# Optimization experiments

Measured on AMD Instinct MI355X. Metric: run time of the kernel, lower is better.

## Reference

```python
import jax, jax.numpy as jnp
import numpy as np

DOMAIN_MIN, DOMAIN_MAX = -1.0, 1.0
N, D_IN, D_OUT, K = 1024, 128, 128, 8


def setup_inputs() -> dict:
    key = jax.random.key(0)
    k1, k2, k3 = jax.random.split(key, 3)
    x = jax.random.uniform(k1, (N, D_IN), dtype=jnp.float32,
                           minval=DOMAIN_MIN, maxval=DOMAIN_MAX)
    # Per-edge spline knot values: near-identity init plus small noise.
    base = jnp.linspace(DOMAIN_MIN, DOMAIN_MAX, K, dtype=jnp.float32)
    coeffs = base[None, None, :] + 0.1 * jax.random.normal(
        k2, (D_OUT, D_IN, K), dtype=jnp.float32)
    weights = jax.random.normal(k3, (D_OUT, D_IN), dtype=jnp.float32) * np.sqrt(2.0 / D_IN)
    bias = jnp.zeros((D_OUT,), dtype=jnp.float32)
    return {"x": x, "coeffs": coeffs, "weights": weights, "bias": bias}


def _spline_all_edges(x, coeffs):
    """Evaluate every edge's cubic (Catmull-Rom) spline at its input.
    x: [N, d_in]; coeffs: [d_out, d_in, K] knot values on uniform knots in [-1,1].
    Returns s: [N, d_in, d_out]."""
    K_ = coeffs.shape[-1]
    h = (DOMAIN_MAX - DOMAIN_MIN) / (K_ - 1)
    xc = jnp.clip(x, DOMAIN_MIN, DOMAIN_MAX)
    t = (xc - DOMAIN_MIN) / h                      # [N, d_in], in [0, K-1]
    idx = jnp.clip(jnp.floor(t).astype(jnp.int32), 0, K_ - 2)
    u = t - idx                                    # local coord in [0,1]
    i0 = jnp.clip(idx - 1, 0, K_ - 1)
    i1 = idx
    i2 = idx + 1
    i3 = jnp.clip(idx + 2, 0, K_ - 1)
    ct = jnp.transpose(coeffs, (1, 2, 0))          # [d_in, K, d_out]
    jar = jnp.arange(ct.shape[0])[None, :]          # [1, d_in]
    p0 = ct[jar, i0]                               # [N, d_in, d_out]
    p1 = ct[jar, i1]
    p2 = ct[jar, i2]
    p3 = ct[jar, i3]
    u2 = u * u
    u3 = u2 * u
    b0 = 0.5 * (-u3 + 2.0 * u2 - u)
    b1 = 0.5 * (3.0 * u3 - 5.0 * u2 + 2.0)
    b2 = 0.5 * (-3.0 * u3 + 4.0 * u2 + u)
    b3 = 0.5 * (u3 - u2)
    return (b0[..., None] * p0 + b1[..., None] * p1 +
            b2[..., None] * p2 + b3[..., None] * p3)


def reference(x, coeffs, weights, bias):
    # h_i(x) = sum_j w_ij * s_ij(x_j) + b_i
    s = _spline_all_edges(x, coeffs)               # [N, d_in, d_out]
    return jnp.einsum('njo,oj->no', s, weights) + bias[None, :]
```

## Files before the change

kernel.cpp:

```cpp
#include <hip/hip_runtime.h>
#include <hip/hip_bf16.h>
#include <stdint.h>


#define DIN 128
#define DOUT 128
#define KTOT 1024
#define MT 16
#define PADW 1032

typedef unsigned int u32;
typedef unsigned short u16;
typedef __attribute__((ext_vector_type(8))) short bf16x8;
typedef __attribute__((ext_vector_type(4))) float f32x4;

union H8 { u16 s[8]; uint4 v; };

__device__ __forceinline__ u16 f2b(float f) {
    union { __hip_bfloat16 h; u16 u; } c;
    c.h = __float2bfloat16(f);
    return c.u;
}

__global__ __launch_bounds__(512) void kan_mfma(
    const float* __restrict__ x, const float* __restrict__ coeffs,
    const float* __restrict__ weights, const float* __restrict__ bias,
    float* __restrict__ out)
{
    __shared__ __align__(16) u16 sA[MT * PADW];
    __shared__ float sC[8 * 256];

    const int tid  = threadIdx.x;
    const int wave = tid >> 6;
    const int lane = tid & 63;
    const int n0 = blockIdx.x * MT;
    const int og = blockIdx.y * 32;

    #pragma unroll
    for (int it = 0; it < 4; ++it) {
        const int task = tid + it * 512;
        const int row = task >> 7;
        const int j = task & 127;
        float xv = x[(n0 + row) * DIN + j];
        xv = fminf(fmaxf(xv, -1.0f), 1.0f);
        const float t = (xv + 1.0f) * 3.5f;
        int idx = (int)t; idx = idx > 6 ? 6 : idx;
        const float u = t - (float)idx;
        const float u2 = u * u, u3 = u2 * u;
        const float b0 = 0.5f * (-u3 + 2.0f * u2 - u);
        const float b1 = 0.5f * (3.0f * u3 - 5.0f * u2 + 2.0f);
        const float b2 = 0.5f * (-3.0f * u3 + 4.0f * u2 + u);
        const float b3 = 0.5f * (u3 - u2);
        float r[8];
        #pragma unroll
        for (int k = 0; k < 8; ++k) r[k] = 0.0f;
        const int i0 = idx > 0 ? idx - 1 : 0;
        const int i3 = idx < 6 ? idx + 2 : 7;
        r[i0] += b0; r[idx] += b1; r[idx + 1] += b2; r[i3] += b3;
        H8 h;
        #pragma unroll
        for (int k = 0; k < 8; ++k) h.s[k] = f2b(r[k]);
        *(uint4*)(sA + row * PADW + j * 8) = h.v;
    }
    __syncthreads();

    const int ot = wave & 1;
    const int kq = wave >> 1;
    const int mo = lane & 15;
    const int q  = lane >> 4;

    const int orow = og + ot * 16 + mo;
    const float* cp = coeffs + orow * KTOT + kq * 256 + q * 8;
    const float* wp = weights + orow * DIN + kq * 32 + q;
    const u16*   ap = sA + mo * PADW + kq * 256 + q * 8;

    f32x4 acc = {0.0f, 0.0f, 0.0f, 0.0f};
    #pragma unroll
    for (int s = 0; s < 8; ++s) {
        bf16x8 af = *(const bf16x8*)(ap + s * 32);
        const float4 c0 = *(const float4*)(cp + s * 32);
        const float4 c1 = *(const float4*)(cp + s * 32 + 4);
        const float wv = wp[s * 4];
        bf16x8 bfr;
        bfr[0] = (short)f2b(c0.x * wv); bfr[1] = (short)f2b(c0.y * wv);
        bfr[2] = (short)f2b(c0.z * wv); bfr[3] = (short)f2b(c0.w * wv);
        bfr[4] = (short)f2b(c1.x * wv); bfr[5] = (short)f2b(c1.y * wv);
        bfr[6] = (short)f2b(c1.z * wv); bfr[7] = (short)f2b(c1.w * wv);
        acc = __builtin_amdgcn_mfma_f32_16x16x32_bf16(af, bfr, acc, 0, 0, 0);
    }

    #pragma unroll
    for (int r = 0; r < 4; ++r)
        sC[wave * 256 + (q * 4 + r) * 16 + mo] = acc[r];
    __syncthreads();

    {
        const int tile = tid >> 8;
        const int idx = tid & 255;
        const int row = idx >> 4, col = idx & 15;
        float v = sC[(0 + tile) * 256 + idx] + sC[(2 + tile) * 256 + idx]
                + sC[(4 + tile) * 256 + idx] + sC[(6 + tile) * 256 + idx];
        const int oc = og + tile * 16 + col;
        out[(n0 + row) * DOUT + oc] = v + bias[oc];
    }
}

extern "C" void kernel_launch(void* const* d_in, const int* in_sizes, int n_in,
                              void* d_out, int out_size, void* d_ws, size_t ws_size,
                              hipStream_t stream) {
    const float* x       = (const float*)d_in[0];
    const float* coeffs  = (const float*)d_in[1];
    const float* weights = (const float*)d_in[2];
    const float* bias    = (const float*)d_in[3];
    float* out = (float*)d_out;
    const int N = in_sizes[0] / DIN;
    dim3 grid(N / MT, DOUT / 32);
    kan_mfma<<<grid, 512, 0, stream>>>(x, coeffs, weights, bias, out);
}
```

Measured before the change: 66.93 us.

## Replace 512-thread shared-memory tiles with one wave per 16x16 output tile

Each workgroup is now a single 64-lane wave that computes one 16x16 output tile over the full K=1024 reduction. The spline basis is built in registers and fed straight into the MFMA, so the LDS staging, the cross-wave partial-sum reduction and both barriers are gone. The grid grows to 512 small blocks. In exchange each wave recomputes basis values for its rows, and the reduction loop per wave is longer, serialising 32 MFMAs on one accumulator.

```diff
diff --git a/kernel.cpp b/kernel.cpp
--- a/kernel.cpp
+++ b/kernel.cpp
@@ -6,15 +6,11 @@
 #define DIN 128
 #define DOUT 128
 #define KTOT 1024
-#define MT 16
-#define PADW 1032
 
 typedef unsigned int u32;
 typedef unsigned short u16;
 typedef __attribute__((ext_vector_type(8))) short bf16x8;
 typedef __attribute__((ext_vector_type(4))) float f32x4;
-
-union H8 { u16 s[8]; uint4 v; };
 
 __device__ __forceinline__ u16 f2b(float f) {
     union { __hip_bfloat16 h; u16 u; } c;
@@ -22,26 +18,31 @@
     return c.u;
 }
 
-__global__ __launch_bounds__(512) void kan_mfma(
+__global__ __launch_bounds__(64) void kan_wave(
     const float* __restrict__ x, const float* __restrict__ coeffs,
     const float* __restrict__ weights, const float* __restrict__ bias,
     float* __restrict__ out)
 {
-    __shared__ __align__(16) u16 sA[MT * PADW];
-    __shared__ float sC[8 * 256];
+    const int lane = threadIdx.x;
+    const int mo = lane & 15;
+    const int q  = lane >> 4;
 
-    const int tid  = threadIdx.x;
-    const int wave = tid >> 6;
-    const int lane = tid & 63;
-    const int n0 = blockIdx.x * MT;
-    const int og = blockIdx.y * 32;
+    const int mt = blockIdx.x & 63;
+    const int ot = blockIdx.x >> 6;
+    const int n0 = mt * 16;
+    const int o0 = ot * 16;
 
-    #pragma unroll
-    for (int it = 0; it < 4; ++it) {
-        const int task = tid + it * 512;
-        const int row = task >> 7;
-        const int j = task & 127;
-        float xv = x[(n0 + row) * DIN + j];
+    const float* xrow = x + (n0 + mo) * DIN;
+    const float* crow = coeffs + (o0 + mo) * KTOT;
+    const float* wrow = weights + (o0 + mo) * DIN;
+
+    f32x4 acc = {0.0f, 0.0f, 0.0f, 0.0f};
+
+    #pragma unroll 8
+    for (int s = 0; s < 32; ++s) {
+        const int j = s * 4 + q;
+
+        float xv = xrow[j];
         xv = fminf(fmaxf(xv, -1.0f), 1.0f);
         const float t = (xv + 1.0f) * 3.5f;
         int idx = (int)t; idx = idx > 6 ? 6 : idx;
@@ -57,52 +58,26 @@
         const int i0 = idx > 0 ? idx - 1 : 0;
         const int i3 = idx < 6 ? idx + 2 : 7;
         r[i0] += b0; r[idx] += b1; r[idx + 1] += b2; r[i3] += b3;
-        H8 h;
+        bf16x8 af;
         #pragma unroll
-        for (int k = 0; k < 8; ++k) h.s[k] = f2b(r[k]);
-        *(uint4*)(sA + row * PADW + j * 8) = h.v;
-    }
-    __syncthreads();
+        for (int k = 0; k < 8; ++k) af[k] = (short)f2b(r[k]);
 
-    const int ot = wave & 1;
-    const int kq = wave >> 1;
-    const int mo = lane & 15;
-    const int q  = lane >> 4;
-
-    const int orow = og + ot * 16 + mo;
-    const float* cp = coeffs + orow * KTOT + kq * 256 + q * 8;
-    const float* wp = weights + orow * DIN + kq * 32 + q;
-    const u16*   ap = sA + mo * PADW + kq * 256 + q * 8;
-
-    f32x4 acc = {0.0f, 0.0f, 0.0f, 0.0f};
-    #pragma unroll
-    for (int s = 0; s < 8; ++s) {
-        bf16x8 af = *(const bf16x8*)(ap + s * 32);
-        const float4 c0 = *(const float4*)(cp + s * 32);
-        const float4 c1 = *(const float4*)(cp + s * 32 + 4);
-        const float wv = wp[s * 4];
+        const float4 c0 = *(const float4*)(crow + j * 8);
+        const float4 c1 = *(const float4*)(crow + j * 8 + 4);
+        const float wv = wrow[j];
         bf16x8 bfr;
         bfr[0] = (short)f2b(c0.x * wv); bfr[1] = (short)f2b(c0.y * wv);
         bfr[2] = (short)f2b(c0.z * wv); bfr[3] = (short)f2b(c0.w * wv);
         bfr[4] = (short)f2b(c1.x * wv); bfr[5] = (short)f2b(c1.y * wv);
         bfr[6] = (short)f2b(c1.z * wv); bfr[7] = (short)f2b(c1.w * wv);
+
         acc = __builtin_amdgcn_mfma_f32_16x16x32_bf16(af, bfr, acc, 0, 0, 0);
     }
 
+    const float bv = bias[o0 + mo];
     #pragma unroll
     for (int r = 0; r < 4; ++r)
-        sC[wave * 256 + (q * 4 + r) * 16 + mo] = acc[r];
-    __syncthreads();
-
-    {
-        const int tile = tid >> 8;
-        const int idx = tid & 255;
-        const int row = idx >> 4, col = idx & 15;
-        float v = sC[(0 + tile) * 256 + idx] + sC[(2 + tile) * 256 + idx]
-                + sC[(4 + tile) * 256 + idx] + sC[(6 + tile) * 256 + idx];
-        const int oc = og + tile * 16 + col;
-        out[(n0 + row) * DOUT + oc] = v + bias[oc];
-    }
+        out[(n0 + q * 4 + r) * DOUT + o0 + mo] = acc[r] + bv;
 }
 
 extern "C" void kernel_launch(void* const* d_in, const int* in_sizes, int n_in,
@@ -114,6 +89,6 @@
     const float* bias    = (const float*)d_in[3];
     float* out = (float*)d_out;
     const int N = in_sizes[0] / DIN;
-    dim3 grid(N / MT, DOUT / 32);
-    kan_mfma<<<grid, 512, 0, stream>>>(x, coeffs, weights, bias, out);
+    kan_wave<<<(N / 16) * (DOUT / 16), 64, 0, stream>>>(
+        x, coeffs, weights, bias, out);
 }
```

Measured after the change: 74.36 us. +11.1%, slower.

## Split into prep kernel writing bf16 basis/weights and a pure MFMA GEMM kernel

Applied to the files above, without the earlier changes.

Splits the fused kernel into two launches. The first computes the bf16 spline-basis matrix and the bf16 weight-scaled coefficients into workspace. The second is a plain MFMA GEMM over 16x16 output tiles that reads both operands from global memory. This removes the redundant per-block recomputation of the basis and of the coefficient conversion, at the cost of a second launch and a round trip of roughly 2.25 MB through global memory.

```diff
diff --git a/kernel.cpp b/kernel.cpp
--- a/kernel.cpp
+++ b/kernel.cpp
@@ -6,8 +6,6 @@
 #define DIN 128
 #define DOUT 128
 #define KTOT 1024
-#define MT 16
-#define PADW 1032
 
 typedef unsigned int u32;
 typedef unsigned short u16;
@@ -22,26 +20,15 @@
     return c.u;
 }
 
-__global__ __launch_bounds__(512) void kan_mfma(
+__global__ __launch_bounds__(256) void kan_prep(
     const float* __restrict__ x, const float* __restrict__ coeffs,
-    const float* __restrict__ weights, const float* __restrict__ bias,
-    float* __restrict__ out)
+    const float* __restrict__ weights, u16* __restrict__ ws0,
+    u16* __restrict__ ws1)
 {
-    __shared__ __align__(16) u16 sA[MT * PADW];
-    __shared__ float sC[8 * 256];
-
-    const int tid  = threadIdx.x;
-    const int wave = tid >> 6;
-    const int lane = tid & 63;
-    const int n0 = blockIdx.x * MT;
-    const int og = blockIdx.y * 32;
-
-    #pragma unroll
-    for (int it = 0; it < 4; ++it) {
-        const int task = tid + it * 512;
-        const int row = task >> 7;
-        const int j = task & 127;
-        float xv = x[(n0 + row) * DIN + j];
+    const int tid = threadIdx.x;
+    if (blockIdx.x < 512) {
+        const int task = blockIdx.x * 256 + tid;
+        float xv = x[task];
         xv = fminf(fmaxf(xv, -1.0f), 1.0f);
         const float t = (xv + 1.0f) * 3.5f;
         int idx = (int)t; idx = idx > 6 ? 6 : idx;
@@ -60,33 +47,44 @@
         H8 h;
         #pragma unroll
         for (int k = 0; k < 8; ++k) h.s[k] = f2b(r[k]);
-        *(uint4*)(sA + row * PADW + j * 8) = h.v;
+        *(uint4*)(ws0 + task * 8) = h.v;
+    } else {
+        const int task = (blockIdx.x - 512) * 256 + tid;
+        const float wv = weights[task];
+        const float4 c0 = *(const float4*)(coeffs + task * 8);
+        const float4 c1 = *(const float4*)(coeffs + task * 8 + 4);
+        H8 h;
+        h.s[0] = f2b(c0.x * wv); h.s[1] = f2b(c0.y * wv);
+        h.s[2] = f2b(c0.z * wv); h.s[3] = f2b(c0.w * wv);
+        h.s[4] = f2b(c1.x * wv); h.s[5] = f2b(c1.y * wv);
+        h.s[6] = f2b(c1.z * wv); h.s[7] = f2b(c1.w * wv);
+        *(uint4*)(ws1 + task * 8) = h.v;
     }
-    __syncthreads();
+}
 
-    const int ot = wave & 1;
-    const int kq = wave >> 1;
+__global__ __launch_bounds__(256) void kan_gemm(
+    const u16* __restrict__ ws0, const u16* __restrict__ ws1,
+    const float* __restrict__ bias, float* __restrict__ out)
+{
+    __shared__ float sC[4 * 256];
+
+    const int tid  = threadIdx.x;
+    const int wave = tid >> 6;
+    const int lane = tid & 63;
     const int mo = lane & 15;
     const int q  = lane >> 4;
+    const int n0 = blockIdx.x * 16;
+    const int o0 = blockIdx.y * 16;
 
-    const int orow = og + ot * 16 + mo;
-    const float* cp = coeffs + orow * KTOT + kq * 256 + q * 8;
-    const float* wp = weights + orow * DIN + kq * 32 + q;
-    const u16*   ap = sA + mo * PADW + kq * 256 + q * 8;
+    const u16* ap = ws0 + (n0 + mo) * KTOT + wave * 256 + q * 8;
+    const u16* bp = ws1 + (o0 + mo) * KTOT + wave * 256 + q * 8;
 
     f32x4 acc = {0.0f, 0.0f, 0.0f, 0.0f};
     #pragma unroll
     for (int s = 0; s < 8; ++s) {
         bf16x8 af = *(const bf16x8*)(ap + s * 32);
-        const float4 c0 = *(const float4*)(cp + s * 32);
-        const float4 c1 = *(const float4*)(cp + s * 32 + 4);
-        const float wv = wp[s * 4];
-        bf16x8 bfr;
-        bfr[0] = (short)f2b(c0.x * wv); bfr[1] = (short)f2b(c0.y * wv);
-        bfr[2] = (short)f2b(c0.z * wv); bfr[3] = (short)f2b(c0.w * wv);
-        bfr[4] = (short)f2b(c1.x * wv); bfr[5] = (short)f2b(c1.y * wv);
-        bfr[6] = (short)f2b(c1.z * wv); bfr[7] = (short)f2b(c1.w * wv);
-        acc = __builtin_amdgcn_mfma_f32_16x16x32_bf16(af, bfr, acc, 0, 0, 0);
+        bf16x8 bf = *(const bf16x8*)(bp + s * 32);
+        acc = __builtin_amdgcn_mfma_f32_16x16x32_bf16(af, bf, acc, 0, 0, 0);
     }
 
     #pragma unroll
@@ -94,15 +92,9 @@
         sC[wave * 256 + (q * 4 + r) * 16 + mo] = acc[r];
     __syncthreads();
 
-    {
-        const int tile = tid >> 8;
-        const int idx = tid & 255;
-        const int row = idx >> 4, col = idx & 15;
-        float v = sC[(0 + tile) * 256 + idx] + sC[(2 + tile) * 256 + idx]
-                + sC[(4 + tile) * 256 + idx] + sC[(6 + tile) * 256 + idx];
-        const int oc = og + tile * 16 + col;
-        out[(n0 + row) * DOUT + oc] = v + bias[oc];
-    }
+    const int row = tid >> 4, col = tid & 15;
+    float v = sC[tid] + sC[256 + tid] + sC[512 + tid] + sC[768 + tid];
+    out[(n0 + row) * DOUT + o0 + col] = v + bias[o0 + col];
 }
 
 extern "C" void kernel_launch(void* const* d_in, const int* in_sizes, int n_in,
@@ -113,7 +105,9 @@
     const float* weights = (const float*)d_in[2];
     const float* bias    = (const float*)d_in[3];
     float* out = (float*)d_out;
-    const int N = in_sizes[0] / DIN;
-    dim3 grid(N / MT, DOUT / 32);
-    kan_mfma<<<grid, 512, 0, stream>>>(x, coeffs, weights, bias, out);
+    u16* ws0 = (u16*)d_ws;
+    u16* ws1 = ws0 + 1024 * KTOT;
+    kan_prep<<<576, 256, 0, stream>>>(x, coeffs, weights, ws0, ws1);
+    dim3 grid(1024 / 16, DOUT / 16);
+    kan_gemm<<<grid, 256, 0, stream>>>(ws0, ws1, bias, out);
 }
```

Result: faster. 65.28 us (-2.5%).
